# Kernel optimization log

Measured on AMD Instinct MI355X. Metric: run time of the kernel, lower is better.

## Reference

```python
import jax, jax.numpy as jnp
import numpy as np
import math

N_HEAD = 16
ROPE_BASE = 10000.0


def _rope_cos_sin(seq_len, head_dim, dtype):
    # standard RoPE tables: freqs_i = base^(-2i/d), i in [0, d/2)
    half = head_dim // 2
    inv_freq = ROPE_BASE ** (-(jnp.arange(half, dtype=jnp.float32) * 2.0 / head_dim))
    t = jnp.arange(seq_len, dtype=jnp.float32)
    ang = t[:, None] * inv_freq[None, :]  # [S, d/2]
    return jnp.cos(ang).astype(dtype), jnp.sin(ang).astype(dtype)


def _apply_rope(x, cos, sin):
    # x: [B, S, H, d]; rotate interleaved even/odd pairs
    x1 = x[..., 0::2]
    x2 = x[..., 1::2]
    c = cos[None, :, None, :]
    s = sin[None, :, None, :]
    out = jnp.stack([x1 * c - x2 * s, x1 * s + x2 * c], axis=-1)
    return out.reshape(x.shape)


def setup_inputs() -> dict:
    key = jax.random.key(0)
    kx, kq, kk, kv, ko = jax.random.split(key, 5)
    B, S, H = 2, 2048, 1024
    x = jax.random.normal(kx, (B, S, H), dtype=jnp.float32)
    scale = 0.02
    w_q = jax.random.normal(kq, (H, H), dtype=jnp.float32) * scale
    w_k = jax.random.normal(kk, (H, H), dtype=jnp.float32) * scale
    w_v = jax.random.normal(kv, (H, H), dtype=jnp.float32) * scale
    w_o = jax.random.normal(ko, (H, H), dtype=jnp.float32) * scale
    return {"x": x, "w_q": w_q, "w_k": w_k, "w_v": w_v, "w_o": w_o}


def reference(x, w_q, w_k, w_v, w_o):
    B, S, H = x.shape
    d = H // N_HEAD
    # torch nn.Linear(bias=False): y = x @ W^T, W is [out, in]
    q = (x @ w_q.T).reshape(B, S, N_HEAD, d)
    k = (x @ w_k.T).reshape(B, S, N_HEAD, d)
    v = (x @ w_v.T).reshape(B, S, N_HEAD, d)
    cos, sin = _rope_cos_sin(S, d, x.dtype)
    q = _apply_rope(q, cos, sin)
    k = _apply_rope(k, cos, sin)
    scores = jnp.einsum("bqhd,bkhd->bhqk", q, k) / math.sqrt(d)
    coefs = jax.nn.softmax(scores, axis=-1)
    # NOTE: causal mask is applied AFTER softmax via tril (no renormalization)
    causal = jnp.tril(jnp.ones((S, S), dtype=bool))
    coefs = jnp.where(causal[None, None], coefs, 0.0)
    out = jnp.einsum("bhqk,bkhd->bqhd", coefs, v).reshape(B, S, H)
    return out @ w_o.T
```

## Files before the change

kernel.cpp:

```cpp
#include <hip/hip_runtime.h>
#include <math.h>

#define SEQ   2048
#define HDIM  1024
#define NH    16
#define DH    64
#define MTOT  4096
#define BHTOT 32

typedef _Float16 half_t;
typedef __attribute__((ext_vector_type(2))) __fp16 fp16x2;
typedef __attribute__((ext_vector_type(4))) _Float16 half4;
typedef __attribute__((ext_vector_type(8))) _Float16 half8;
typedef __attribute__((ext_vector_type(4))) float float4v;

typedef __attribute__((address_space(1))) const unsigned int guint;
typedef __attribute__((address_space(3))) unsigned int luint;
__device__ __forceinline__ void glds16(const half_t* g, half_t* l) {
    __builtin_amdgcn_global_load_lds((guint*)g, (luint*)l, 16, 0, 0);
}

__global__ __launch_bounds__(256)
void prep(const float* __restrict__ x,  const float* __restrict__ wq,
          const float* __restrict__ wk, const float* __restrict__ wv,
          const float* __restrict__ wo,
          half_t* __restrict__ xh,  half_t* __restrict__ wqh,
          half_t* __restrict__ wkh, half_t* __restrict__ wvh,
          half_t* __restrict__ woh, float2* __restrict__ rope)
{
    const int bid = blockIdx.x;
    if (bid < 8192) {
        int i = bid * 256 + threadIdx.x;
        const float* s; half_t* d;
        if (i < 1048576) { s = x; d = xh; }
        else {
            int j = i - 1048576;
            int w = j >> 18; i = j & 262143;
            s = (w == 0) ? wq : (w == 1) ? wk : (w == 2) ? wv : wo;
            d = (w == 0) ? wqh : (w == 1) ? wkh : (w == 2) ? wvh : woh;
        }
        float4 v = ((const float4*)s)[i];
        union { half_t h[4]; uint2 u; } tmp;
        tmp.h[0] = (half_t)v.x; tmp.h[1] = (half_t)v.y;
        tmp.h[2] = (half_t)v.z; tmp.h[3] = (half_t)v.w;
        ((uint2*)d)[i] = tmp.u;
    } else {
        int tt = (bid - 8192) * 256 + threadIdx.x;
        int s = tt >> 5, j = tt & 31;
        float inv = powf(10000.0f, -(float)j / 32.0f);
        float ang = (float)s * inv;
        rope[tt] = make_float2(cosf(ang), sinf(ang));
    }
}

__global__ __launch_bounds__(256, 5)
void gemm_qkv(const half_t* __restrict__ A,
              const half_t* __restrict__ w0, const half_t* __restrict__ w1,
              const half_t* __restrict__ w2,
              half_t* __restrict__ Qb, half_t* __restrict__ Kb,
              half_t* __restrict__ Vtb,
              const float2* __restrict__ rope)
{
    const int mode = blockIdx.z;
    const half_t* Bw = (mode == 1) ? w1 : (mode == 2) ? w2 : w0;

    __shared__ __align__(16) half_t Tsh[2][128][64];
    half_t (*Ash)[64] = Tsh[0];
    half_t (*Bsh)[64] = Tsh[1];

    const int t    = threadIdx.x;
    const int lane = t & 63;
    const int wave = t >> 6;
    const int quad = lane >> 4;
    const int l16  = lane & 15;
    const int wr   = (wave >> 1) * 64;
    const int wc   = (wave & 1) * 64;
    const int bm   = blockIdx.x, bn = blockIdx.y;

    const int srow   = lane >> 3;
    const int schunk = (lane & 7) ^ (srow & 3);
    const half_t* Asrc = A  + (size_t)(bm * 128 + srow) * HDIM + schunk * 8;
    const half_t* Bsrc = Bw + (size_t)(bn * 128 + srow) * HDIM + schunk * 8;
    const int swz = (l16 & 3) << 4;

    float4v acc[4][4] = {};

    for (int kt = 0; kt < HDIM / 64; ++kt) {
        const half_t* Ak = Asrc + kt * 64;
        const half_t* Bk = Bsrc + kt * 64;
#pragma unroll
        for (int c = 0; c < 4; ++c) {
            const int r8 = wave * 32 + c * 8;
            glds16(Ak + (size_t)r8 * HDIM, &Ash[r8][0]);
            glds16(Bk + (size_t)r8 * HDIM, &Bsh[r8][0]);
        }
        __syncthreads();
#pragma unroll
        for (int kk = 0; kk < 2; ++kk) {
            const int cb = ((quad << 4) | (kk << 6)) ^ swz;
            half8 af[4], bf[4];
#pragma unroll
            for (int mb = 0; mb < 4; ++mb)
                af[mb] = *(const half8*)((const char*)&Ash[wr + mb * 16 + l16][0] + cb);
#pragma unroll
            for (int nb = 0; nb < 4; ++nb)
                bf[nb] = *(const half8*)((const char*)&Bsh[wc + nb * 16 + l16][0] + cb);
#pragma unroll
            for (int mb = 0; mb < 4; ++mb)
#pragma unroll
                for (int nb = 0; nb < 4; ++nb)
                    acc[mb][nb] = __builtin_amdgcn_mfma_f32_16x16x32_f16(af[mb], bf[nb], acc[mb][nb], 0, 0, 0);
        }
        __syncthreads();
    }

    if (mode == 2) {
#pragma unroll
        for (int mb = 0; mb < 4; ++mb)
#pragma unroll
            for (int nb = 0; nb < 4; ++nb) {
                int row0 = bm * 128 + wr + mb * 16 + quad * 4;
                int col  = bn * 128 + wc + nb * 16 + l16;
                int b = row0 >> 11, s0 = row0 & 2047;
                int h = col >> 6,  dd = col & 63;
                union { half_t h4[4]; uint2 u; } tmp;
#pragma unroll
                for (int r = 0; r < 4; ++r) tmp.h4[r] = (half_t)acc[mb][nb][r];
                *(uint2*)&Vtb[((size_t)((b * NH + h) * DH + dd)) * SEQ + s0] = tmp.u;
            }
        return;
    }
    {
        half_t* Ob = (mode == 0) ? Qb : Kb;
        const float scl = (mode == 0) ? 0.125f * 1.44269504088896f : 1.0f;
        const int h = (bn * 128 + wc) >> 6;
        float* E = (float*)&Tsh[0][0][0] + wave * 1088;
#pragma unroll
        for (int mb = 0; mb < 4; ++mb) {
#pragma unroll
            for (int nb = 0; nb < 4; ++nb)
#pragma unroll
                for (int r = 0; r < 4; ++r)
                    E[(quad * 4 + r) * 68 + nb * 16 + l16] = acc[mb][nb][r];
            __asm__ volatile("s_waitcnt lgkmcnt(0)" ::: "memory");
#pragma unroll
            for (int c = 0; c < 2; ++c) {
                const int uidx = c * 64 + lane;
                const int row = uidx >> 3, ch = uidx & 7;
                const int sg = bm * 128 + wr + mb * 16 + row;
                const int b = sg >> 11, s = sg & 2047;
                const float* Er = E + row * 68 + ch * 8;
                const float4 e0 = *(const float4*)Er;
                const float4 e1 = *(const float4*)(Er + 4);
                const float4* rp = (const float4*)(rope + (size_t)s * 32 + ch * 4);
                const float4 r01 = rp[0];
                const float4 r23 = rp[1];
                union { half_t hh[8]; uint4 u; } o;
                o.hh[0] = (half_t)((e0.x * r01.x - e0.y * r01.y) * scl);
                o.hh[1] = (half_t)((e0.x * r01.y + e0.y * r01.x) * scl);
                o.hh[2] = (half_t)((e0.z * r01.z - e0.w * r01.w) * scl);
                o.hh[3] = (half_t)((e0.z * r01.w + e0.w * r01.z) * scl);
                o.hh[4] = (half_t)((e1.x * r23.x - e1.y * r23.y) * scl);
                o.hh[5] = (half_t)((e1.x * r23.y + e1.y * r23.x) * scl);
                o.hh[6] = (half_t)((e1.z * r23.z - e1.w * r23.w) * scl);
                o.hh[7] = (half_t)((e1.z * r23.w + e1.w * r23.z) * scl);
                *(uint4*)&Ob[((size_t)((b * NH + h) * SEQ + s)) * DH + ch * 8] = o.u;
            }
        }
    }
}

__global__ __launch_bounds__(256)
void gemm_out(const half_t* __restrict__ A, const half_t* __restrict__ W,
              float* __restrict__ outF)
{
    __shared__ __align__(16) half_t Ash[2][64][64];
    __shared__ __align__(16) half_t Bsh[2][128][64];

    const int t    = threadIdx.x;
    const int lane = t & 63;
    const int wave = t >> 6;
    const int quad = lane >> 4;
    const int l16  = lane & 15;
    const int wr   = (wave >> 1) * 32;
    const int wc   = (wave & 1) * 64;
    const int bm   = blockIdx.x, bn = blockIdx.y;

    const int srow   = lane >> 3;
    const int schunk = (lane & 7) ^ (srow & 3);
    const half_t* Asrc = A + (size_t)(bm * 64  + srow) * HDIM + schunk * 8;
    const half_t* Bsrc = W + (size_t)(bn * 128 + srow) * HDIM + schunk * 8;
    const int swz = (l16 & 3) << 4;

    auto stage = [&](int kt, int buf) {
        const half_t* Ak = Asrc + kt * 64;
        const half_t* Bk = Bsrc + kt * 64;
#pragma unroll
        for (int c = 0; c < 2; ++c) {
            const int r8 = wave * 16 + c * 8;
            glds16(Ak + (size_t)r8 * HDIM, &Ash[buf][r8][0]);
        }
#pragma unroll
        for (int c = 0; c < 4; ++c) {
            const int r8 = wave * 32 + c * 8;
            glds16(Bk + (size_t)r8 * HDIM, &Bsh[buf][r8][0]);
        }
    };

    float4v acc[2][4] = {};

    stage(0, 0);
    __asm__ volatile("s_waitcnt vmcnt(0)" ::: "memory");
    __builtin_amdgcn_s_barrier();
    __builtin_amdgcn_sched_barrier(0);

    for (int kt = 0; kt < HDIM / 64; ++kt) {
        const int cur = kt & 1, nxt = cur ^ 1;
        if (kt + 1 < HDIM / 64) stage(kt + 1, nxt);
#pragma unroll
        for (int kk = 0; kk < 2; ++kk) {
            const int cb = ((quad << 4) | (kk << 6)) ^ swz;
            half8 af[2], bf[4];
#pragma unroll
            for (int mb = 0; mb < 2; ++mb)
                af[mb] = *(const half8*)((const char*)&Ash[cur][wr + mb * 16 + l16][0] + cb);
#pragma unroll
            for (int nb = 0; nb < 4; ++nb)
                bf[nb] = *(const half8*)((const char*)&Bsh[cur][wc + nb * 16 + l16][0] + cb);
#pragma unroll
            for (int mb = 0; mb < 2; ++mb)
#pragma unroll
                for (int nb = 0; nb < 4; ++nb)
                    acc[mb][nb] = __builtin_amdgcn_mfma_f32_16x16x32_f16(af[mb], bf[nb], acc[mb][nb], 0, 0, 0);
        }
        __asm__ volatile("s_waitcnt vmcnt(0)" ::: "memory");
        __builtin_amdgcn_s_barrier();
        __builtin_amdgcn_sched_barrier(0);
    }

#pragma unroll
    for (int mb = 0; mb < 2; ++mb)
#pragma unroll
        for (int nb = 0; nb < 4; ++nb) {
            int row0 = bm * 64 + wr + mb * 16 + quad * 4;
            int col  = bn * 128 + wc + nb * 16 + l16;
#pragma unroll
            for (int r = 0; r < 4; ++r)
                outF[(size_t)(row0 + r) * HDIM + col] = acc[mb][nb][r];
        }
}

__global__ __launch_bounds__(512, 4)
void attn_fused(const half_t* __restrict__ Qb, const half_t* __restrict__ Kb,
                const half_t* __restrict__ Vtb, half_t* __restrict__ AOut)
{
    const int bx = blockIdx.x;
    const int p  = bx >> 1;
    const int hf = bx & 1;
    const int bh = blockIdx.y;
    const int NT = SEQ / 64;

    __shared__ __align__(16) half_t Ksh[3][64][64];
    __shared__ __align__(16) half_t Vsh[2][64][64];

    const int t = threadIdx.x;
    const int wave = t >> 6, lane = t & 63, quad = lane >> 4, l16 = lane & 15;
    const int heavy = wave >> 2, wl = wave & 3;
    const int qtile = heavy ? (15 - p) : p;
    const int q0 = qtile * 128 + hf * 64 + wl * 16;
    const int ktop = 2 * (15 - p) + hf;

    const half_t* Qp = Qb + ((size_t)bh * SEQ + q0 + l16) * DH + quad * 8;
    const half8 qf0 = *(const half8*)Qp;
    const half8 qf1 = *(const half8*)(Qp + 32);

    float4v o[4] = {};
    float4v ls = {};

    const int krow = lane >> 3, kpos = lane & 7;
    const int kchunk = kpos ^ krow;
    const half_t* Ksrc = Kb + ((size_t)bh * SEQ + wave * 8 + krow) * DH + kchunk * 8;
    const int ko1 = ((quad ^ (l16 & 7)) * 8);
    const int ko2 = ko1 ^ 32;

    const int sr  = t >> 3;
    const int svc = ((t & 7) ^ (sr & 7)) * 8;
    const half_t* Vg = Vtb + ((size_t)bh * DH + sr) * SEQ + (t & 7) * 8;
    const int vxo = l16 & 7;
    const int vro = (quad & 1) * 8;

    uint4 va = *(const uint4*)(Vg);
    glds16(Ksrc,                   &Ksh[0][wave * 8][0]);
    glds16(Ksrc + (size_t)64 * DH, &Ksh[1][wave * 8][0]);
    *(uint4*)&Vsh[0][sr][svc] = va;
    __asm__ volatile("s_waitcnt vmcnt(1)" ::: "memory");
    __asm__ volatile("s_waitcnt lgkmcnt(0)" ::: "memory");
    __builtin_amdgcn_s_barrier();
    __builtin_amdgcn_sched_barrier(0);

    int i0 = 0, i1 = 1, i2 = 2;
    for (int kt = 0; kt < NT; ++kt) {
        const int curv = kt & 1, nxtv = curv ^ 1;
        const bool vnext = (kt + 1 <= ktop) && (kt + 1 < NT);
        const bool knext = (kt + 2 < NT);

        if (vnext) va = *(const uint4*)(Vg + (kt + 1) * 64);
        if (knext)
            glds16(Ksrc + (size_t)(kt + 2) * 64 * DH, &Ksh[i2][wave * 8][0]);

        float4v sc[4];
        __builtin_amdgcn_s_setprio(1);
#pragma unroll
        for (int nb = 0; nb < 4; ++nb) {
            const half_t* kp = &Ksh[i0][nb * 16 + l16][0];
            half8 kf0 = *(const half8*)(kp + ko1);
            half8 kf1 = *(const half8*)(kp + ko2);
            float4v a = {};
            a = __builtin_amdgcn_mfma_f32_16x16x32_f16(kf0, qf0, a, 0, 0, 0);
            a = __builtin_amdgcn_mfma_f32_16x16x32_f16(kf1, qf1, a, 0, 0, 0);
            sc[nb] = a;
        }
        __builtin_amdgcn_s_setprio(0);

#pragma unroll
        for (int nb = 0; nb < 4; ++nb)
#pragma unroll
            for (int r = 0; r < 4; ++r) {
                float e = __builtin_amdgcn_exp2f(sc[nb][r]);
                sc[nb][r] = e;
                ls[r] += e;
            }

        const int kbase = kt * 64;
        if (kbase <= q0 + 15) {
            if (kbase + 63 > q0) {
                int qg = q0 + l16;
#pragma unroll
                for (int nb = 0; nb < 4; ++nb)
#pragma unroll
                    for (int r = 0; r < 4; ++r)
                        if (kbase + nb * 16 + quad * 4 + r > qg) sc[nb][r] = 0.f;
            }
            half4 pf[4];
#pragma unroll
            for (int nb = 0; nb < 4; ++nb) {
                union { fp16x2 v2[2]; half4 v4; } u;
                u.v2[0] = __builtin_amdgcn_cvt_pkrtz(sc[nb][0], sc[nb][1]);
                u.v2[1] = __builtin_amdgcn_cvt_pkrtz(sc[nb][2], sc[nb][3]);
                pf[nb] = u.v4;
            }
            __builtin_amdgcn_s_setprio(1);
#pragma unroll
            for (int md = 0; md < 4; ++md) {
                const char* vrow = (const char*)&Vsh[curv][md * 16 + l16][0];
#pragma unroll
                for (int nb = 0; nb < 4; ++nb) {
                    const int sco = (((nb * 2 + (quad >> 1)) ^ vxo) << 4) + vro;
                    half4 vf = *(const half4*)(vrow + sco);
                    o[md] = __builtin_amdgcn_mfma_f32_16x16x16f16(vf, pf[nb], o[md], 0, 0, 0);
                }
            }
            __builtin_amdgcn_s_setprio(0);
        }

        if (vnext) *(uint4*)&Vsh[nxtv][sr][svc] = va;
        if (knext) { __asm__ volatile("s_waitcnt vmcnt(1)" ::: "memory"); }
        else       { __asm__ volatile("s_waitcnt vmcnt(0)" ::: "memory"); }
        __asm__ volatile("s_waitcnt lgkmcnt(0)" ::: "memory");
        __builtin_amdgcn_s_barrier();
        __builtin_amdgcn_sched_barrier(0);
        const int tmp = i0; i0 = i1; i1 = i2; i2 = tmp;
    }

    const int b = bh >> 4, h = bh & 15;
    const int orow = lane >> 2, occ = (lane & 3) * 16;
    half_t* scr = (heavy ? (half_t*)Vsh : (half_t*)Ksh) + wl * 1152;
    half_t (*Osh)[72] = (half_t(*)[72])scr;
    {
        float rs = (ls[0] + ls[1]) + (ls[2] + ls[3]);
        rs += __shfl_xor(rs, 16, 64);
        rs += __shfl_xor(rs, 32, 64);
        const float inv = 1.0f / rs;
#pragma unroll
        for (int md = 0; md < 4; ++md)
#pragma unroll
            for (int r = 0; r < 4; ++r)
                Osh[l16][md * 16 + quad * 4 + r] = (half_t)(o[md][r] * inv);
        __asm__ volatile("s_waitcnt lgkmcnt(0)" ::: "memory");
        uint4 o0 = *(const uint4*)&Osh[orow][occ];
        uint4 o1 = *(const uint4*)&Osh[orow][occ + 8];
        const int s = q0 + orow;
        half_t* dst = AOut + ((size_t)(b * SEQ + s)) * HDIM + h * DH + occ;
        *(uint4*)dst       = o0;
        *(uint4*)(dst + 8) = o1;
    }
}

extern "C" void kernel_launch(void* const* d_in, const int* in_sizes, int n_in,
                              void* d_out, int out_size, void* d_ws, size_t ws_size,
                              hipStream_t stream)
{
    const float* x  = (const float*)d_in[0];
    const float* wq = (const float*)d_in[1];
    const float* wk = (const float*)d_in[2];
    const float* wv = (const float*)d_in[3];
    const float* wo = (const float*)d_in[4];
    float* out = (float*)d_out;

    char* ws = (char*)d_ws;
    size_t off = 0;
    auto alloc = [&](size_t bytes) -> void* {
        void* p = ws + off;
        off += (bytes + 255) & ~(size_t)255;
        return p;
    };
    half_t* xh   = (half_t*)alloc((size_t)MTOT * HDIM * 2);
    half_t* wqh  = (half_t*)alloc((size_t)HDIM * HDIM * 2);
    half_t* wkh  = (half_t*)alloc((size_t)HDIM * HDIM * 2);
    half_t* wvh  = (half_t*)alloc((size_t)HDIM * HDIM * 2);
    half_t* woh  = (half_t*)alloc((size_t)HDIM * HDIM * 2);
    half_t* Qb   = (half_t*)alloc((size_t)BHTOT * SEQ * DH * 2);
    half_t* Kb   = (half_t*)alloc((size_t)BHTOT * SEQ * DH * 2);
    half_t* Vtb  = (half_t*)alloc((size_t)BHTOT * SEQ * DH * 2);
    half_t* ah   = (half_t*)alloc((size_t)MTOT * HDIM * 2);
    float2* rope = (float2*)alloc((size_t)SEQ * 32 * sizeof(float2));

    prep<<<8448, 256, 0, stream>>>(x, wq, wk, wv, wo, xh, wqh, wkh, wvh, woh, rope);

    gemm_qkv<<<dim3(32, 8, 3), 256, 0, stream>>>(xh, wqh, wkh, wvh,
                                                 Qb, Kb, Vtb, rope);
    attn_fused<<<dim3(16, 32), 512, 0, stream>>>(Qb, Kb, Vtb, ah);
    gemm_out<<<dim3(64, 8), 256, 0, stream>>>(ah, woh, out);
}
```

Before: 188.7 us.

## Software-pipeline QK^T ahead of PV in attention and shrink out-proj tile

The attention loop is restructured so the QK^T scores and softmax for the next key tile are computed while the PV MMA runs on the current tile. It keeps three K buffers in flight and ping-pongs two probability register sets across an unrolled-by-two loop. Separately, the output projection GEMM tile is narrowed from 64x128 to 64x64, doubling its grid for better CU occupancy at the cost of more redundant A loads. The pipelining raises register pressure and makes the prefetch and barrier logic more complex.

```diff
diff --git a/kernel.cpp b/kernel.cpp
--- a/kernel.cpp
+++ b/kernel.cpp
@@ -175,7 +175,7 @@
               float* __restrict__ outF)
 {
     __shared__ __align__(16) half_t Ash[2][64][64];
-    __shared__ __align__(16) half_t Bsh[2][128][64];
+    __shared__ __align__(16) half_t Bsh[2][64][64];
 
     const int t    = threadIdx.x;
     const int lane = t & 63;
@@ -183,13 +183,13 @@
     const int quad = lane >> 4;
     const int l16  = lane & 15;
     const int wr   = (wave >> 1) * 32;
-    const int wc   = (wave & 1) * 64;
+    const int wc   = (wave & 1) * 32;
     const int bm   = blockIdx.x, bn = blockIdx.y;
 
     const int srow   = lane >> 3;
     const int schunk = (lane & 7) ^ (srow & 3);
-    const half_t* Asrc = A + (size_t)(bm * 64  + srow) * HDIM + schunk * 8;
-    const half_t* Bsrc = W + (size_t)(bn * 128 + srow) * HDIM + schunk * 8;
+    const half_t* Asrc = A + (size_t)(bm * 64 + srow) * HDIM + schunk * 8;
+    const half_t* Bsrc = W + (size_t)(bn * 64 + srow) * HDIM + schunk * 8;
     const int swz = (l16 & 3) << 4;
 
     auto stage = [&](int kt, int buf) {
@@ -199,15 +199,11 @@
         for (int c = 0; c < 2; ++c) {
             const int r8 = wave * 16 + c * 8;
             glds16(Ak + (size_t)r8 * HDIM, &Ash[buf][r8][0]);
-        }
-#pragma unroll
-        for (int c = 0; c < 4; ++c) {
-            const int r8 = wave * 32 + c * 8;
             glds16(Bk + (size_t)r8 * HDIM, &Bsh[buf][r8][0]);
         }
     };
 
-    float4v acc[2][4] = {};
+    float4v acc[2][2] = {};
 
     stage(0, 0);
     __asm__ volatile("s_waitcnt vmcnt(0)" ::: "memory");
@@ -220,17 +216,17 @@
 #pragma unroll
         for (int kk = 0; kk < 2; ++kk) {
             const int cb = ((quad << 4) | (kk << 6)) ^ swz;
-            half8 af[2], bf[4];
+            half8 af[2], bf[2];
 #pragma unroll
             for (int mb = 0; mb < 2; ++mb)
                 af[mb] = *(const half8*)((const char*)&Ash[cur][wr + mb * 16 + l16][0] + cb);
 #pragma unroll
-            for (int nb = 0; nb < 4; ++nb)
+            for (int nb = 0; nb < 2; ++nb)
                 bf[nb] = *(const half8*)((const char*)&Bsh[cur][wc + nb * 16 + l16][0] + cb);
 #pragma unroll
             for (int mb = 0; mb < 2; ++mb)
 #pragma unroll
-                for (int nb = 0; nb < 4; ++nb)
+                for (int nb = 0; nb < 2; ++nb)
                     acc[mb][nb] = __builtin_amdgcn_mfma_f32_16x16x32_f16(af[mb], bf[nb], acc[mb][nb], 0, 0, 0);
         }
         __asm__ volatile("s_waitcnt vmcnt(0)" ::: "memory");
@@ -241,9 +237,9 @@
 #pragma unroll
     for (int mb = 0; mb < 2; ++mb)
 #pragma unroll
-        for (int nb = 0; nb < 4; ++nb) {
+        for (int nb = 0; nb < 2; ++nb) {
             int row0 = bm * 64 + wr + mb * 16 + quad * 4;
-            int col  = bn * 128 + wc + nb * 16 + l16;
+            int col  = bn * 64 + wc + nb * 16 + l16;
 #pragma unroll
             for (int r = 0; r < 4; ++r)
                 outF[(size_t)(row0 + r) * HDIM + col] = acc[mb][nb][r];
@@ -289,30 +285,24 @@
     const int vxo = l16 & 7;
     const int vro = (quad & 1) * 8;
 
-    uint4 va = *(const uint4*)(Vg);
-    glds16(Ksrc,                   &Ksh[0][wave * 8][0]);
-    glds16(Ksrc + (size_t)64 * DH, &Ksh[1][wave * 8][0]);
-    *(uint4*)&Vsh[0][sr][svc] = va;
+    {
+        uint4 va = *(const uint4*)(Vg);
+        glds16(Ksrc,                       &Ksh[0][wave * 8][0]);
+        glds16(Ksrc + (size_t)64 * DH,     &Ksh[1][wave * 8][0]);
+        glds16(Ksrc + (size_t)2 * 64 * DH, &Ksh[2][wave * 8][0]);
+        *(uint4*)&Vsh[0][sr][svc] = va;
+    }
     __asm__ volatile("s_waitcnt vmcnt(1)" ::: "memory");
     __asm__ volatile("s_waitcnt lgkmcnt(0)" ::: "memory");
     __builtin_amdgcn_s_barrier();
     __builtin_amdgcn_sched_barrier(0);
 
-    int i0 = 0, i1 = 1, i2 = 2;
-    for (int kt = 0; kt < NT; ++kt) {
-        const int curv = kt & 1, nxtv = curv ^ 1;
-        const bool vnext = (kt + 1 <= ktop) && (kt + 1 < NT);
-        const bool knext = (kt + 2 < NT);
-
-        if (vnext) va = *(const uint4*)(Vg + (kt + 1) * 64);
-        if (knext)
-            glds16(Ksrc + (size_t)(kt + 2) * 64 * DH, &Ksh[i2][wave * 8][0]);
-
+    half4 pfA[4], pfB[4];
+    {
         float4v sc[4];
-        __builtin_amdgcn_s_setprio(1);
 #pragma unroll
         for (int nb = 0; nb < 4; ++nb) {
-            const half_t* kp = &Ksh[i0][nb * 16 + l16][0];
+            const half_t* kp = &Ksh[0][nb * 16 + l16][0];
             half8 kf0 = *(const half8*)(kp + ko1);
             half8 kf1 = *(const half8*)(kp + ko2);
             float4v a = {};
@@ -320,8 +310,6 @@
             a = __builtin_amdgcn_mfma_f32_16x16x32_f16(kf1, qf1, a, 0, 0, 0);
             sc[nb] = a;
         }
-        __builtin_amdgcn_s_setprio(0);
-
 #pragma unroll
         for (int nb = 0; nb < 4; ++nb)
 #pragma unroll
@@ -330,25 +318,55 @@
                 sc[nb][r] = e;
                 ls[r] += e;
             }
-
-        const int kbase = kt * 64;
-        if (kbase <= q0 + 15) {
-            if (kbase + 63 > q0) {
-                int qg = q0 + l16;
-#pragma unroll
-                for (int nb = 0; nb < 4; ++nb)
-#pragma unroll
-                    for (int r = 0; r < 4; ++r)
-                        if (kbase + nb * 16 + quad * 4 + r > qg) sc[nb][r] = 0.f;
-            }
-            half4 pf[4];
+        if (63 > q0) {
+            int qg = q0 + l16;
+#pragma unroll
+            for (int nb = 0; nb < 4; ++nb)
+#pragma unroll
+                for (int r = 0; r < 4; ++r)
+                    if (nb * 16 + quad * 4 + r > qg) sc[nb][r] = 0.f;
+        }
+#pragma unroll
+        for (int nb = 0; nb < 4; ++nb) {
+            union { fp16x2 v2[2]; half4 v4; } u;
+            u.v2[0] = __builtin_amdgcn_cvt_pkrtz(sc[nb][0], sc[nb][1]);
+            u.v2[1] = __builtin_amdgcn_cvt_pkrtz(sc[nb][2], sc[nb][3]);
+            pfA[nb] = u.v4;
+        }
+    }
+    __builtin_amdgcn_s_barrier();
+    __builtin_amdgcn_sched_barrier(0);
+
+    int a0 = 0, a1 = 1, a2 = 2;
+
+    auto iter = [&](int tk, half4 (&pfP)[4], half4 (&pfC)[4]) {
+        const bool vnext = (tk + 1 <= ktop) && (tk + 1 < NT);
+        const bool k3    = (tk + 3 < NT);
+        const int curv = tk & 1, nxtv = curv ^ 1;
+
+        uint4 van;
+        if (vnext) van = *(const uint4*)(Vg + (tk + 1) * 64);
+        if (k3)
+            glds16(Ksrc + (size_t)(tk + 3) * 64 * DH, &Ksh[a0][wave * 8][0]);
+
+        const bool qk = (tk + 1 < NT);
+        float4v sc[4];
+        if (qk) {
+            __builtin_amdgcn_s_setprio(1);
 #pragma unroll
             for (int nb = 0; nb < 4; ++nb) {
-                union { fp16x2 v2[2]; half4 v4; } u;
-                u.v2[0] = __builtin_amdgcn_cvt_pkrtz(sc[nb][0], sc[nb][1]);
-                u.v2[1] = __builtin_amdgcn_cvt_pkrtz(sc[nb][2], sc[nb][3]);
-                pf[nb] = u.v4;
-            }
+                const half_t* kp = &Ksh[a1][nb * 16 + l16][0];
+                half8 kf0 = *(const half8*)(kp + ko1);
+                half8 kf1 = *(const half8*)(kp + ko2);
+                float4v a = {};
+                a = __builtin_amdgcn_mfma_f32_16x16x32_f16(kf0, qf0, a, 0, 0, 0);
+                a = __builtin_amdgcn_mfma_f32_16x16x32_f16(kf1, qf1, a, 0, 0, 0);
+                sc[nb] = a;
+            }
+            __builtin_amdgcn_s_setprio(0);
+        }
+
+        if (tk * 64 <= q0 + 15) {
             __builtin_amdgcn_s_setprio(1);
 #pragma unroll
             for (int md = 0; md < 4; ++md) {
@@ -357,19 +375,53 @@
                 for (int nb = 0; nb < 4; ++nb) {
                     const int sco = (((nb * 2 + (quad >> 1)) ^ vxo) << 4) + vro;
                     half4 vf = *(const half4*)(vrow + sco);
-                    o[md] = __builtin_amdgcn_mfma_f32_16x16x16f16(vf, pf[nb], o[md], 0, 0, 0);
+                    o[md] = __builtin_amdgcn_mfma_f32_16x16x16f16(vf, pfP[nb], o[md], 0, 0, 0);
                 }
             }
             __builtin_amdgcn_s_setprio(0);
         }
 
-        if (vnext) *(uint4*)&Vsh[nxtv][sr][svc] = va;
-        if (knext) { __asm__ volatile("s_waitcnt vmcnt(1)" ::: "memory"); }
-        else       { __asm__ volatile("s_waitcnt vmcnt(0)" ::: "memory"); }
+        if (qk) {
+#pragma unroll
+            for (int nb = 0; nb < 4; ++nb)
+#pragma unroll
+                for (int r = 0; r < 4; ++r) {
+                    float e = __builtin_amdgcn_exp2f(sc[nb][r]);
+                    sc[nb][r] = e;
+                    ls[r] += e;
+                }
+            const int kbase = (tk + 1) * 64;
+            if (kbase <= q0 + 15) {
+                if (kbase + 63 > q0) {
+                    int qg = q0 + l16;
+#pragma unroll
+                    for (int nb = 0; nb < 4; ++nb)
+#pragma unroll
+                        for (int r = 0; r < 4; ++r)
+                            if (kbase + nb * 16 + quad * 4 + r > qg) sc[nb][r] = 0.f;
+                }
+#pragma unroll
+                for (int nb = 0; nb < 4; ++nb) {
+                    union { fp16x2 v2[2]; half4 v4; } u;
+                    u.v2[0] = __builtin_amdgcn_cvt_pkrtz(sc[nb][0], sc[nb][1]);
+                    u.v2[1] = __builtin_amdgcn_cvt_pkrtz(sc[nb][2], sc[nb][3]);
+                    pfC[nb] = u.v4;
+                }
+            }
+        }
+
+        if (vnext) *(uint4*)&Vsh[nxtv][sr][svc] = van;
+        if (k3) { __asm__ volatile("s_waitcnt vmcnt(1)" ::: "memory"); }
+        else    { __asm__ volatile("s_waitcnt vmcnt(0)" ::: "memory"); }
         __asm__ volatile("s_waitcnt lgkmcnt(0)" ::: "memory");
         __builtin_amdgcn_s_barrier();
         __builtin_amdgcn_sched_barrier(0);
-        const int tmp = i0; i0 = i1; i1 = i2; i2 = tmp;
+        const int tmp = a0; a0 = a1; a1 = a2; a2 = tmp;
+    };
+
+    for (int tk = 0; tk < NT; tk += 2) {
+        iter(tk,     pfA, pfB);
+        iter(tk + 1, pfB, pfA);
     }
 
     const int b = bh >> 4, h = bh & 15;
@@ -430,5 +482,5 @@
     gemm_qkv<<<dim3(32, 8, 3), 256, 0, stream>>>(xh, wqh, wkh, wvh,
                                                  Qb, Kb, Vtb, rope);
     attn_fused<<<dim3(16, 32), 512, 0, stream>>>(Qb, Kb, Vtb, ah);
-    gemm_out<<<dim3(64, 8), 256, 0, stream>>>(ah, woh, out);
-}
+    gemm_out<<<dim3(64, 16), 256, 0, stream>>>(ah, woh, out);
+}
```

Result: no change. 186.3 us (-1.3%).

## Use 128-key tiles in attention and 64x64 tiles in output GEMM

Applied to the files above, without the earlier changes.

The attention kernel now stages 128-key K/V tiles per iteration with a double buffer instead of 64-key tiles with a triple-buffered K. This halves the number of barriers and loop iterations, and the V layout and swizzle are changed to fit the wider tile. The output projection GEMM drops from 64x128 to 64x64 tiles, doubling the grid to raise occupancy and parallelism at the cost of loading the A operand twice as often. The wider attention tile adds shared memory per block, which may lower occupancy, and each K prefetch now has less lookahead.

```diff
diff --git a/kernel.cpp b/kernel.cpp
--- a/kernel.cpp
+++ b/kernel.cpp
@@ -175,7 +175,7 @@
               float* __restrict__ outF)
 {
     __shared__ __align__(16) half_t Ash[2][64][64];
-    __shared__ __align__(16) half_t Bsh[2][128][64];
+    __shared__ __align__(16) half_t Bsh[2][64][64];
 
     const int t    = threadIdx.x;
     const int lane = t & 63;
@@ -183,13 +183,13 @@
     const int quad = lane >> 4;
     const int l16  = lane & 15;
     const int wr   = (wave >> 1) * 32;
-    const int wc   = (wave & 1) * 64;
+    const int wc   = (wave & 1) * 32;
     const int bm   = blockIdx.x, bn = blockIdx.y;
 
     const int srow   = lane >> 3;
     const int schunk = (lane & 7) ^ (srow & 3);
-    const half_t* Asrc = A + (size_t)(bm * 64  + srow) * HDIM + schunk * 8;
-    const half_t* Bsrc = W + (size_t)(bn * 128 + srow) * HDIM + schunk * 8;
+    const half_t* Asrc = A + (size_t)(bm * 64 + srow) * HDIM + schunk * 8;
+    const half_t* Bsrc = W + (size_t)(bn * 64 + srow) * HDIM + schunk * 8;
     const int swz = (l16 & 3) << 4;
 
     auto stage = [&](int kt, int buf) {
@@ -199,15 +199,11 @@
         for (int c = 0; c < 2; ++c) {
             const int r8 = wave * 16 + c * 8;
             glds16(Ak + (size_t)r8 * HDIM, &Ash[buf][r8][0]);
-        }
-#pragma unroll
-        for (int c = 0; c < 4; ++c) {
-            const int r8 = wave * 32 + c * 8;
             glds16(Bk + (size_t)r8 * HDIM, &Bsh[buf][r8][0]);
         }
     };
 
-    float4v acc[2][4] = {};
+    float4v acc[2][2] = {};
 
     stage(0, 0);
     __asm__ volatile("s_waitcnt vmcnt(0)" ::: "memory");
@@ -220,17 +216,17 @@
 #pragma unroll
         for (int kk = 0; kk < 2; ++kk) {
             const int cb = ((quad << 4) | (kk << 6)) ^ swz;
-            half8 af[2], bf[4];
+            half8 af[2], bf[2];
 #pragma unroll
             for (int mb = 0; mb < 2; ++mb)
                 af[mb] = *(const half8*)((const char*)&Ash[cur][wr + mb * 16 + l16][0] + cb);
 #pragma unroll
-            for (int nb = 0; nb < 4; ++nb)
+            for (int nb = 0; nb < 2; ++nb)
                 bf[nb] = *(const half8*)((const char*)&Bsh[cur][wc + nb * 16 + l16][0] + cb);
 #pragma unroll
             for (int mb = 0; mb < 2; ++mb)
 #pragma unroll
-                for (int nb = 0; nb < 4; ++nb)
+                for (int nb = 0; nb < 2; ++nb)
                     acc[mb][nb] = __builtin_amdgcn_mfma_f32_16x16x32_f16(af[mb], bf[nb], acc[mb][nb], 0, 0, 0);
         }
         __asm__ volatile("s_waitcnt vmcnt(0)" ::: "memory");
@@ -241,9 +237,9 @@
 #pragma unroll
     for (int mb = 0; mb < 2; ++mb)
 #pragma unroll
-        for (int nb = 0; nb < 4; ++nb) {
+        for (int nb = 0; nb < 2; ++nb) {
             int row0 = bm * 64 + wr + mb * 16 + quad * 4;
-            int col  = bn * 128 + wc + nb * 16 + l16;
+            int col  = bn * 64 + wc + nb * 16 + l16;
 #pragma unroll
             for (int r = 0; r < 4; ++r)
                 outF[(size_t)(row0 + r) * HDIM + col] = acc[mb][nb][r];
@@ -258,17 +254,17 @@
     const int p  = bx >> 1;
     const int hf = bx & 1;
     const int bh = blockIdx.y;
-    const int NT = SEQ / 64;
-
-    __shared__ __align__(16) half_t Ksh[3][64][64];
-    __shared__ __align__(16) half_t Vsh[2][64][64];
+    const int NT = SEQ / 128;
+
+    __shared__ __align__(16) half_t Ksh[2][128][64];
+    __shared__ __align__(16) half_t Vsh[2][64][128];
 
     const int t = threadIdx.x;
     const int wave = t >> 6, lane = t & 63, quad = lane >> 4, l16 = lane & 15;
     const int heavy = wave >> 2, wl = wave & 3;
     const int qtile = heavy ? (15 - p) : p;
     const int q0 = qtile * 128 + hf * 64 + wl * 16;
-    const int ktop = 2 * (15 - p) + hf;
+    const int vtop = 15 - p;
 
     const half_t* Qp = Qb + ((size_t)bh * SEQ + q0 + l16) * DH + quad * 8;
     const half8 qf0 = *(const half8*)Qp;
@@ -279,97 +275,111 @@
 
     const int krow = lane >> 3, kpos = lane & 7;
     const int kchunk = kpos ^ krow;
-    const half_t* Ksrc = Kb + ((size_t)bh * SEQ + wave * 8 + krow) * DH + kchunk * 8;
+    const half_t* Ksrc = Kb + ((size_t)bh * SEQ + wave * 16 + krow) * DH + kchunk * 8;
     const int ko1 = ((quad ^ (l16 & 7)) * 8);
     const int ko2 = ko1 ^ 32;
 
     const int sr  = t >> 3;
-    const int svc = ((t & 7) ^ (sr & 7)) * 8;
-    const half_t* Vg = Vtb + ((size_t)bh * DH + sr) * SEQ + (t & 7) * 8;
-    const int vxo = l16 & 7;
-    const int vro = (quad & 1) * 8;
-
-    uint4 va = *(const uint4*)(Vg);
-    glds16(Ksrc,                   &Ksh[0][wave * 8][0]);
-    glds16(Ksrc + (size_t)64 * DH, &Ksh[1][wave * 8][0]);
-    *(uint4*)&Vsh[0][sr][svc] = va;
-    __asm__ volatile("s_waitcnt vmcnt(1)" ::: "memory");
+    const int sc0 = t & 7;
+    const half_t* Vg = Vtb + ((size_t)bh * DH + sr) * SEQ + sc0 * 8;
+    const int vso0 = ((sc0    ) ^ (sr & 15)) * 8;
+    const int vso1 = ((sc0 + 8) ^ (sr & 15)) * 8;
+
+    {
+        uint4 va0 = *(const uint4*)(Vg);
+        uint4 va1 = *(const uint4*)(Vg + 64);
+        glds16(Ksrc,          &Ksh[0][wave * 16][0]);
+        glds16(Ksrc + 8 * DH, &Ksh[0][wave * 16 + 8][0]);
+        *(uint4*)&Vsh[0][sr][vso0] = va0;
+        *(uint4*)&Vsh[0][sr][vso1] = va1;
+    }
+    __asm__ volatile("s_waitcnt vmcnt(0)" ::: "memory");
     __asm__ volatile("s_waitcnt lgkmcnt(0)" ::: "memory");
     __builtin_amdgcn_s_barrier();
     __builtin_amdgcn_sched_barrier(0);
 
-    int i0 = 0, i1 = 1, i2 = 2;
-    for (int kt = 0; kt < NT; ++kt) {
-        const int curv = kt & 1, nxtv = curv ^ 1;
-        const bool vnext = (kt + 1 <= ktop) && (kt + 1 < NT);
-        const bool knext = (kt + 2 < NT);
-
-        if (vnext) va = *(const uint4*)(Vg + (kt + 1) * 64);
-        if (knext)
-            glds16(Ksrc + (size_t)(kt + 2) * 64 * DH, &Ksh[i2][wave * 8][0]);
-
-        float4v sc[4];
-        __builtin_amdgcn_s_setprio(1);
-#pragma unroll
-        for (int nb = 0; nb < 4; ++nb) {
-            const half_t* kp = &Ksh[i0][nb * 16 + l16][0];
-            half8 kf0 = *(const half8*)(kp + ko1);
-            half8 kf1 = *(const half8*)(kp + ko2);
-            float4v a = {};
-            a = __builtin_amdgcn_mfma_f32_16x16x32_f16(kf0, qf0, a, 0, 0, 0);
-            a = __builtin_amdgcn_mfma_f32_16x16x32_f16(kf1, qf1, a, 0, 0, 0);
-            sc[nb] = a;
-        }
-        __builtin_amdgcn_s_setprio(0);
-
-#pragma unroll
-        for (int nb = 0; nb < 4; ++nb)
-#pragma unroll
-            for (int r = 0; r < 4; ++r) {
-                float e = __builtin_amdgcn_exp2f(sc[nb][r]);
-                sc[nb][r] = e;
-                ls[r] += e;
-            }
-
-        const int kbase = kt * 64;
-        if (kbase <= q0 + 15) {
-            if (kbase + 63 > q0) {
-                int qg = q0 + l16;
-#pragma unroll
-                for (int nb = 0; nb < 4; ++nb)
-#pragma unroll
-                    for (int r = 0; r < 4; ++r)
-                        if (kbase + nb * 16 + quad * 4 + r > qg) sc[nb][r] = 0.f;
-            }
-            half4 pf[4];
+    for (int T = 0; T < NT; ++T) {
+        const int cur = T & 1, nxt = cur ^ 1;
+        const bool kn = (T + 1 < NT);
+        const bool vn = kn && (T + 1 <= vtop);
+
+        uint4 va0, va1;
+        if (vn) {
+            va0 = *(const uint4*)(Vg + (T + 1) * 128);
+            va1 = *(const uint4*)(Vg + (T + 1) * 128 + 64);
+        }
+        if (kn) {
+            const half_t* Kn = Ksrc + (size_t)(T + 1) * 128 * DH;
+            glds16(Kn,          &Ksh[nxt][wave * 16][0]);
+            glds16(Kn + 8 * DH, &Ksh[nxt][wave * 16 + 8][0]);
+        }
+
+#pragma unroll
+        for (int hh = 0; hh < 2; ++hh) {
+            float4v sc[4];
+            __builtin_amdgcn_s_setprio(1);
 #pragma unroll
             for (int nb = 0; nb < 4; ++nb) {
-                union { fp16x2 v2[2]; half4 v4; } u;
-                u.v2[0] = __builtin_amdgcn_cvt_pkrtz(sc[nb][0], sc[nb][1]);
-                u.v2[1] = __builtin_amdgcn_cvt_pkrtz(sc[nb][2], sc[nb][3]);
-                pf[nb] = u.v4;
-            }
-            __builtin_amdgcn_s_setprio(1);
-#pragma unroll
-            for (int md = 0; md < 4; ++md) {
-                const char* vrow = (const char*)&Vsh[curv][md * 16 + l16][0];
-#pragma unroll
-                for (int nb = 0; nb < 4; ++nb) {
-                    const int sco = (((nb * 2 + (quad >> 1)) ^ vxo) << 4) + vro;
-                    half4 vf = *(const half4*)(vrow + sco);
-                    o[md] = __builtin_amdgcn_mfma_f32_16x16x16f16(vf, pf[nb], o[md], 0, 0, 0);
-                }
+                const half_t* kp = &Ksh[cur][hh * 64 + nb * 16 + l16][0];
+                half8 kf0 = *(const half8*)(kp + ko1);
+                half8 kf1 = *(const half8*)(kp + ko2);
+                float4v a = {};
+                a = __builtin_amdgcn_mfma_f32_16x16x32_f16(kf0, qf0, a, 0, 0, 0);
+                a = __builtin_amdgcn_mfma_f32_16x16x32_f16(kf1, qf1, a, 0, 0, 0);
+                sc[nb] = a;
             }
             __builtin_amdgcn_s_setprio(0);
-        }
-
-        if (vnext) *(uint4*)&Vsh[nxtv][sr][svc] = va;
-        if (knext) { __asm__ volatile("s_waitcnt vmcnt(1)" ::: "memory"); }
-        else       { __asm__ volatile("s_waitcnt vmcnt(0)" ::: "memory"); }
+
+#pragma unroll
+            for (int nb = 0; nb < 4; ++nb)
+#pragma unroll
+                for (int r = 0; r < 4; ++r) {
+                    float e = __builtin_amdgcn_exp2f(sc[nb][r]);
+                    sc[nb][r] = e;
+                    ls[r] += e;
+                }
+
+            const int kbase = T * 128 + hh * 64;
+            if (kbase <= q0 + 15) {
+                if (kbase + 63 > q0) {
+                    int qg = q0 + l16;
+#pragma unroll
+                    for (int nb = 0; nb < 4; ++nb)
+#pragma unroll
+                        for (int r = 0; r < 4; ++r)
+                            if (kbase + nb * 16 + quad * 4 + r > qg) sc[nb][r] = 0.f;
+                }
+                half4 pf[4];
+#pragma unroll
+                for (int nb = 0; nb < 4; ++nb) {
+                    union { fp16x2 v2[2]; half4 v4; } u;
+                    u.v2[0] = __builtin_amdgcn_cvt_pkrtz(sc[nb][0], sc[nb][1]);
+                    u.v2[1] = __builtin_amdgcn_cvt_pkrtz(sc[nb][2], sc[nb][3]);
+                    pf[nb] = u.v4;
+                }
+                __builtin_amdgcn_s_setprio(1);
+#pragma unroll
+                for (int md = 0; md < 4; ++md) {
+                    const char* vrow = (const char*)&Vsh[cur][md * 16 + l16][0];
+#pragma unroll
+                    for (int nb = 0; nb < 4; ++nb) {
+                        const int chunk = (hh * 8 + nb * 2 + (quad >> 1)) ^ l16;
+                        half4 vf = *(const half4*)(vrow + chunk * 16 + (quad & 1) * 8);
+                        o[md] = __builtin_amdgcn_mfma_f32_16x16x16f16(vf, pf[nb], o[md], 0, 0, 0);
+                    }
+                }
+                __builtin_amdgcn_s_setprio(0);
+            }
+        }
+
+        if (vn) {
+            *(uint4*)&Vsh[nxt][sr][vso0] = va0;
+            *(uint4*)&Vsh[nxt][sr][vso1] = va1;
+        }
+        __asm__ volatile("s_waitcnt vmcnt(0)" ::: "memory");
         __asm__ volatile("s_waitcnt lgkmcnt(0)" ::: "memory");
         __builtin_amdgcn_s_barrier();
         __builtin_amdgcn_sched_barrier(0);
-        const int tmp = i0; i0 = i1; i1 = i2; i2 = tmp;
     }
 
     const int b = bh >> 4, h = bh & 15;
@@ -430,5 +440,5 @@
     gemm_qkv<<<dim3(32, 8, 3), 256, 0, stream>>>(xh, wqh, wkh, wvh,
                                                  Qb, Kb, Vtb, rope);
     attn_fused<<<dim3(16, 32), 512, 0, stream>>>(Qb, Kb, Vtb, ah);
-    gemm_out<<<dim3(64, 8), 256, 0, stream>>>(ah, woh, out);
-}
+    gemm_out<<<dim3(64, 16), 256, 0, stream>>>(ah, woh, out);
+}
```

Result: no change. 186.6 us (-1.1%).
